# Optimization experiments

Hardware: AMD Instinct MI355X
Metric: run time of the kernel (lower is better)

## Reference

```python
import jax, jax.numpy as jnp
import numpy as np

B, MAX_S, HID = 128, 4096, 5120
H, D_NOPE, D_ROPE, D_V = 128, 128, 64, 128
KV_SIZE = 512 + 64  # kv_lora_rank + qk_rope_head_dim = 576


def setup_inputs() -> dict:
    key = jax.random.key(0)
    ks = jax.random.split(key, 8)
    seq_lens = jax.random.randint(ks[0], (B,), 1, MAX_S)
    return {
        "hidden_states": jax.random.normal(ks[1], (B, 1, HID), jnp.float32),
        "k_cache": jax.random.normal(ks[2], (B, MAX_S, D_NOPE), jnp.float32),
        "v_cache": jax.random.normal(ks[3], (B, MAX_S, D_V), jnp.float32),
        "Wq": jax.random.normal(ks[4], (HID, H * (D_NOPE + D_ROPE)), jnp.float32) * 0.02,
        "Wkv": jax.random.normal(ks[5], (HID, KV_SIZE), jnp.float32) * 0.02,
        "Wo": jax.random.normal(ks[6], (H * D_V, HID), jnp.float32) * 0.02,
        "positions": seq_lens - 1,
        "slot_mapping": seq_lens - 1,
        "seq_lens": seq_lens,
    }


def reference(hidden_states, k_cache, v_cache, Wq, Wkv, Wo, positions, slot_mapping, seq_lens):
    h = hidden_states[:, -1, :]                        # [B, HID] last-token decode
    q = (h @ Wq).reshape(B, H, D_NOPE + D_ROPE)        # [B, H, 192]
    kv = h @ Wkv                                       # [B, 576]
    q_nope = q[:, :, :D_NOPE]                          # [B, H, 128]
    k_new = kv[:, :D_NOPE]                             # [B, 128]
    v_new = kv[:, D_NOPE:D_NOPE + D_V]                 # [B, 128]

    b_idx = jnp.arange(B)
    kc = k_cache.at[b_idx, slot_mapping].set(k_new)    # write new token into paged cache
    vc = v_cache.at[b_idx, slot_mapping].set(v_new)

    scale = D_NOPE ** -0.5
    scores = jnp.einsum('bhd,bsd->bhs', q_nope, kc) * scale  # MQA: 1 kv head broadcast
    valid = jnp.arange(MAX_S)[None, :] < seq_lens[:, None]   # [B, S]
    scores = jnp.where(valid[:, None, :], scores, jnp.float32(-1e30))
    p = jax.nn.softmax(scores, axis=-1)
    attn = jnp.einsum('bhs,bsd->bhd', p, vc)           # [B, H, 128]

    return attn.reshape(B, 1, H * D_V) @ Wo            # [B, 1, HID]
```

## Files before the change

### kernel.cpp

```cpp
#include <hip/hip_runtime.h>
#include <hip/hip_bf16.h>

typedef __attribute__((ext_vector_type(4))) float f32x4;
typedef __attribute__((ext_vector_type(8))) short bf16x8;
typedef __attribute__((ext_vector_type(2))) unsigned int u32x2;
typedef __attribute__((ext_vector_type(4))) unsigned int u32x4;

static __device__ __forceinline__ unsigned short f2bf(float f) {
    unsigned u = __builtin_bit_cast(unsigned, f);
    u += 0x7fffu + ((u >> 16) & 1u);
    return (unsigned short)(u >> 16);
}
static __device__ __forceinline__ unsigned pack2(float a, float b) {
    __hip_bfloat162 h = __float22bfloat162_rn(make_float2(a, b));
    unsigned u;
    __builtin_memcpy(&u, &h, 4);
    return u;
}
static __device__ __forceinline__ float bf2f(unsigned short s) {
    unsigned u = (unsigned)s << 16;
    float f;
    __builtin_memcpy(&f, &u, 4);
    return f;
}

static __device__ __forceinline__ void bar_nodrain() {
    __builtin_amdgcn_sched_barrier(0);
    asm volatile("s_waitcnt lgkmcnt(0)" ::: "memory");
    __builtin_amdgcn_s_barrier();
    __builtin_amdgcn_sched_barrier(0);
}

__global__ __launch_bounds__(256)
void cvt_bf16(const float* __restrict__ in, unsigned* __restrict__ out, int n8)
{
    const int i = blockIdx.x * 256 + threadIdx.x;
    if (i >= n8) return;
    f32x4 a = ((const f32x4*)in)[2 * i];
    f32x4 b = ((const f32x4*)in)[2 * i + 1];
    u32x4 p = { pack2(a[0], a[1]), pack2(a[2], a[3]), pack2(b[0], b[1]), pack2(b[2], b[3]) };
    ((u32x4*)out)[i] = p;
}

template<int CBF16, int COLMAP>
__device__ __forceinline__
void gemm_body(const unsigned short* __restrict__ Ah, int lda,
               const float* __restrict__ Bm, int ldb,
               void* __restrict__ Cp, int ldc,
               int kchunk, int nsplit, int bidx,
               unsigned short* As, unsigned short* Bs)
{
    const int tid = threadIdx.x;
    const int w = tid >> 6, l = tid & 63, lg = l >> 4, l15 = l & 15;
    const int bx = bidx / nsplit;
    const int by = bidx % nsplit;
    const int n0 = bx * 64;
    const int pcol = COLMAP ? ((n0 >> 7) * 192 + (n0 & 127)) : n0;
    const size_t k0base = (size_t)by * (size_t)kchunk;

    const int ar = tid >> 1;
    const int ac = (tid & 1) * 32;
    const int bnb = (tid & 15) * 4;
    const int bkk = tid >> 4;

    u32x4 aReg[4];
    f32x4 b0Reg[2][2], b1Reg[2][2];

    auto loadA = [&](size_t k0) {
#pragma unroll
        for (int k = 0; k < 4; k++)
            aReg[k] = *(const u32x4*)(Ah + (size_t)ar * lda + k0 + ac + 8 * k);
    };
    auto storeA = [&]() {
#pragma unroll
        for (int k = 0; k < 4; k++)
            *(u32x4*)&As[ar * 72 + ac + 8 * k] = aReg[k];
    };
    auto loadB = [&](f32x4 (&bR)[2][2], size_t k0) {
#pragma unroll
        for (int i = 0; i < 2; i++) {
            const float* bp = Bm + (k0 + (size_t)(2 * (bkk + 16 * i))) * (size_t)ldb + pcol + bnb;
            bR[i][0] = *(const f32x4*)bp;
            bR[i][1] = *(const f32x4*)(bp + ldb);
        }
    };
    auto storeB = [&](f32x4 (&bR)[2][2]) {
        unsigned* bd = (unsigned*)Bs;
#pragma unroll
        for (int i = 0; i < 2; i++)
#pragma unroll
            for (int j = 0; j < 4; j++)
                bd[(bnb + j) * 33 + bkk + 16 * i] = pack2(bR[i][0][j], bR[i][1][j]);
    };

    f32x4 acc[2][4];
    const f32x4 fzero = {0.f, 0.f, 0.f, 0.f};
#pragma unroll
    for (int a = 0; a < 2; a++)
#pragma unroll
        for (int b2 = 0; b2 < 4; b2++) acc[a][b2] = fzero;

    auto mfmaStep = [&]() {
#pragma unroll
        for (int ks = 0; ks < 2; ks++) {
            bf16x8 bfr[4];
#pragma unroll
            for (int nf = 0; nf < 4; nf++)
                bfr[nf] = *(const bf16x8*)&Bs[(16 * nf + l15) * 66 + 32 * ks + 8 * lg];
#pragma unroll
            for (int mf = 0; mf < 2; mf++) {
                bf16x8 af = *(const bf16x8*)&As[(32 * w + 16 * mf + l15) * 72 + 32 * ks + 8 * lg];
#pragma unroll
                for (int nf = 0; nf < 4; nf++)
                    acc[mf][nf] = __builtin_amdgcn_mfma_f32_16x16x32_bf16(af, bfr[nf], acc[mf][nf], 0, 0, 0);
            }
        }
    };

    const int nst = kchunk >> 6;
    auto kof = [&](int t) { return k0base + (size_t)(t << 6); };

    loadA(kof(0));
    loadB(b0Reg, kof(0));
    if (nst > 1) loadB(b1Reg, kof(1));

    for (int t = 0; t < nst; t += 2) {
        storeA(); storeB(b0Reg);
        bar_nodrain();
        if (t + 1 < nst) loadA(kof(t + 1));
        if (t + 2 < nst) loadB(b0Reg, kof(t + 2));
        __builtin_amdgcn_sched_barrier(0);
        mfmaStep();
        bar_nodrain();
        if (t + 1 < nst) {
            storeA(); storeB(b1Reg);
            bar_nodrain();
            if (t + 2 < nst) loadA(kof(t + 2));
            if (t + 3 < nst) loadB(b1Reg, kof(t + 3));
            __builtin_amdgcn_sched_barrier(0);
            mfmaStep();
            bar_nodrain();
        }
    }
#pragma unroll
    for (int mf = 0; mf < 2; mf++) {
#pragma unroll
        for (int nf = 0; nf < 4; nf++) {
            const int m0 = 32 * w + 16 * mf + 4 * lg;
            const int cn = n0 + 16 * nf + l15;
            if (CBF16) {
                unsigned short* Ch = (unsigned short*)Cp + (size_t)by * ((size_t)128 * (size_t)ldc);
#pragma unroll
                for (int r = 0; r < 4; r++)
                    Ch[(size_t)(m0 + r) * ldc + cn] = f2bf(acc[mf][nf][r]);
            } else {
                float* Cf = (float*)Cp + (size_t)by * ((size_t)128 * (size_t)ldc);
#pragma unroll
                for (int r = 0; r < 4; r++)
                    Cf[(size_t)(m0 + r) * ldc + cn] = acc[mf][nf][r];
            }
        }
    }
}

#define QBLOCKS 1024

__global__ __launch_bounds__(256, 4)
void proj_fused(const unsigned short* __restrict__ hb,
                const float* __restrict__ Wq, const float* __restrict__ Wkv,
                unsigned short* __restrict__ qp, float* __restrict__ kvp)
{
    __shared__ __align__(16) unsigned short As[128 * 72];
    __shared__ __align__(16) unsigned short Bs[64 * 66];
    if (blockIdx.x < QBLOCKS)
        gemm_body<1, 1>(hb, 5120, Wq, 24576, qp, 16384, 1280, 4, blockIdx.x, As, Bs);
    else
        gemm_body<0, 0>(hb, 5120, Wkv, 576, kvp, 256, 320, 16, blockIdx.x - QBLOCKS, As, Bs);
}

__global__ __launch_bounds__(256, 4)
void gemm_out(const unsigned short* __restrict__ Ah, const float* __restrict__ Wo,
              unsigned short* __restrict__ outp)
{
    __shared__ __align__(16) unsigned short As[128 * 72];
    __shared__ __align__(16) unsigned short Bs[64 * 66];
    gemm_body<1, 0>(Ah, 16384, Wo, 5120, outp, 5120, 1024, 16, blockIdx.x, As, Bs);
}

__global__ __launch_bounds__(256)
void reduce_q_bf16(const unsigned short* __restrict__ in, unsigned* __restrict__ out)
{
    const int i = blockIdx.x * 256 + threadIdx.x;
    const u32x4* in4 = (const u32x4*)in;
    u32x4 v0 = in4[i];
    u32x4 v1 = in4[i + 262144];
    u32x4 v2 = in4[i + 2 * 262144];
    u32x4 v3 = in4[i + 3 * 262144];
    const float scale = 0.088388347648318447f;
    u32x4 r;
#pragma unroll
    for (int wd = 0; wd < 4; wd++) {
        float lo = bf2f((unsigned short)(v0[wd] & 0xffff)) + bf2f((unsigned short)(v1[wd] & 0xffff))
                 + bf2f((unsigned short)(v2[wd] & 0xffff)) + bf2f((unsigned short)(v3[wd] & 0xffff));
        float hi = bf2f((unsigned short)(v0[wd] >> 16)) + bf2f((unsigned short)(v1[wd] >> 16))
                 + bf2f((unsigned short)(v2[wd] >> 16)) + bf2f((unsigned short)(v3[wd] >> 16));
        r[wd] = pack2(lo * scale, hi * scale);
    }
    ((u32x4*)out)[i] = r;
}

#define NSPLIT 8
#define CHUNK_T 8
#define KVSPLIT 16

__global__ __launch_bounds__(512, 4)
void attn_fwd(const float* __restrict__ kc, const float* __restrict__ vc,
              const unsigned short* __restrict__ qb, const float* __restrict__ kvp,
              const int* __restrict__ seq_lens, const int* __restrict__ slot_map,
              unsigned short* __restrict__ Opart, float* __restrict__ m_ws, float* __restrict__ l_ws)
{
    __shared__ __align__(16) unsigned short Ks [64 * 136];
    __shared__ __align__(16) unsigned short Vts[128 * 72];
    __shared__ __align__(16) unsigned short Ps [128 * 72];
    __shared__ float knew_s[128];
    __shared__ float vnew_s[128];

    const int b = blockIdx.x, split = blockIdx.y;
    const int seq = seq_lens[b], slot = slot_map[b];
    const int nt = (seq + 63) >> 6;
    const int t0 = split * CHUNK_T;
    const int t1 = min(t0 + CHUNK_T, nt);
    const int slotTile = slot >> 6;

    const int tid = threadIdx.x, w = tid >> 6, l = tid & 63, lg = l >> 4, l15 = l & 15;
    const int h = 16 * w + l15;

    float m_run = -__builtin_inff(), l_run = 0.0f;

    if (t0 < t1) {
        if (slotTile >= t0 && slotTile < t1 && tid < 256) {
            float s = 0.f;
#pragma unroll
            for (int j = 0; j < KVSPLIT; j++) s += kvp[j * 32768 + b * 256 + tid];
            if (tid < 128) knew_s[tid] = s;
            else           vnew_s[tid - 128] = s;
        }

        bf16x8 qf[4];
        {
            const unsigned short* qrow = qb + (size_t)b * 16384 + (size_t)h * 128;
#pragma unroll
            for (int ks = 0; ks < 4; ks++)
                qf[ks] = *(const bf16x8*)(qrow + 32 * ks + 8 * lg);
        }

        f32x4 kReg[4];
        f32x4 vReg[2][2];
        const int kr  = tid >> 3;
        const int kcb = (tid & 7) * 16;
        const int vsp = tid & 31;
        const int vdq = tid >> 5;

        auto loadKV = [&](int t) {
            const int s0 = t << 6;
            const float* ksrc = kc + ((size_t)b * 4096 + s0 + kr) * 128 + kcb;
#pragma unroll
            for (int c = 0; c < 4; c++) kReg[c] = *(const f32x4*)(ksrc + 4 * c);
#pragma unroll
            for (int i = 0; i < 2; i++) {
                const int d4 = 4 * vdq + 64 * i;
                const float* r1 = vc + ((size_t)b * 4096 + s0 + 2 * vsp) * 128 + d4;
                vReg[i][0] = *(const f32x4*)r1;
                vReg[i][1] = *(const f32x4*)(r1 + 128);
            }
        };
        auto storeKV = [&]() {
            u32x4 w0 = { pack2(kReg[0][0], kReg[0][1]), pack2(kReg[0][2], kReg[0][3]),
                         pack2(kReg[1][0], kReg[1][1]), pack2(kReg[1][2], kReg[1][3]) };
            u32x4 w1 = { pack2(kReg[2][0], kReg[2][1]), pack2(kReg[2][2], kReg[2][3]),
                         pack2(kReg[3][0], kReg[3][1]), pack2(kReg[3][2], kReg[3][3]) };
            *(u32x4*)&Ks[kr * 136 + kcb] = w0;
            *(u32x4*)&Ks[kr * 136 + kcb + 8] = w1;
            unsigned* vt = (unsigned*)Vts;
#pragma unroll
            for (int i = 0; i < 2; i++)
#pragma unroll
                for (int j = 0; j < 4; j++)
                    vt[(4 * vdq + 64 * i + j) * 36 + vsp] = pack2(vReg[i][0][j], vReg[i][1][j]);
        };

        f32x4 accO[8];
        const f32x4 fzero = {0.f, 0.f, 0.f, 0.f};
#pragma unroll
        for (int i = 0; i < 8; i++) accO[i] = fzero;

        loadKV(t0);
        for (int t = t0; t < t1; ++t) {
            const int s0 = t << 6;
            storeKV();
            bar_nodrain();
            if (t == slotTile) {
                if (tid < 128) {
                    const int sloc = slot & 63;
                    Ks [sloc * 136 + tid] = f2bf(knew_s[tid]);
                    Vts[tid * 72 + sloc]  = f2bf(vnew_s[tid]);
                }
                bar_nodrain();
            }
            if (t + 1 < t1) loadKV(t + 1);
            __builtin_amdgcn_sched_barrier(0);

            f32x4 accS[4];
#pragma unroll
            for (int sf = 0; sf < 4; sf++) accS[sf] = fzero;
#pragma unroll
            for (int ks = 0; ks < 4; ks++) {
#pragma unroll
                for (int sf = 0; sf < 4; sf++) {
                    bf16x8 kf = *(const bf16x8*)&Ks[(16 * sf + l15) * 136 + 32 * ks + 8 * lg];
                    accS[sf] = __builtin_amdgcn_mfma_f32_16x16x32_bf16(kf, qf[ks], accS[sf], 0, 0, 0);
                }
            }
            float tmax = -__builtin_inff();
#pragma unroll
            for (int sf = 0; sf < 4; sf++) {
#pragma unroll
                for (int r = 0; r < 4; r++) {
                    const int s = s0 + 16 * sf + 4 * lg + r;
                    float sc = (s < seq) ? accS[sf][r] : -__builtin_inff();
                    accS[sf][r] = sc;
                    tmax = fmaxf(tmax, sc);
                }
            }
            tmax = fmaxf(tmax, __shfl_xor(tmax, 16));
            tmax = fmaxf(tmax, __shfl_xor(tmax, 32));
            const float mnew = fmaxf(m_run, tmax);
            const float so = __expf(m_run - mnew);
            float lsum = 0.f;
#pragma unroll
            for (int sf = 0; sf < 4; sf++) {
#pragma unroll
                for (int r = 0; r < 4; r++) {
                    const float p = __expf(accS[sf][r] - mnew);
                    accS[sf][r] = p;
                    lsum += p;
                }
            }
            lsum += __shfl_xor(lsum, 16);
            lsum += __shfl_xor(lsum, 32);
            l_run = l_run * so + lsum;
            m_run = mnew;
#pragma unroll
            for (int i = 0; i < 8; i++) accO[i] *= so;

            {
                unsigned* pd = (unsigned*)Ps;
#pragma unroll
                for (int sf = 0; sf < 4; sf++) {
                    pd[h * 36 + 8 * sf + 2 * lg + 0] = pack2(accS[sf][0], accS[sf][1]);
                    pd[h * 36 + 8 * sf + 2 * lg + 1] = pack2(accS[sf][2], accS[sf][3]);
                }
            }
            bf16x8 pf[2];
#pragma unroll
            for (int ks = 0; ks < 2; ks++)
                pf[ks] = *(const bf16x8*)&Ps[h * 72 + 32 * ks + 8 * lg];
#pragma unroll
            for (int df = 0; df < 8; df++) {
#pragma unroll
                for (int ks = 0; ks < 2; ks++) {
                    bf16x8 vf = *(const bf16x8*)&Vts[(16 * df + l15) * 72 + 32 * ks + 8 * lg];
                    accO[df] = __builtin_amdgcn_mfma_f32_16x16x32_bf16(vf, pf[ks], accO[df], 0, 0, 0);
                }
            }
            bar_nodrain();
        }
        unsigned short* ob = Opart + ((size_t)(b * NSPLIT + split)) * 16384 + (size_t)h * 128;
#pragma unroll
        for (int df = 0; df < 8; df++) {
            u32x2 p = { pack2(accO[df][0], accO[df][1]), pack2(accO[df][2], accO[df][3]) };
            *(u32x2*)&ob[16 * df + 4 * lg] = p;
        }
    }
    if (lg == 0) {
        m_ws[(b * NSPLIT + split) * 128 + h] = m_run;
        l_ws[(b * NSPLIT + split) * 128 + h] = l_run;
    }
}

__global__ __launch_bounds__(256)
void combine8(const unsigned short* __restrict__ Opart, const float* __restrict__ m_ws,
              const float* __restrict__ l_ws, unsigned* __restrict__ attn_bf)
{
    const int idx = blockIdx.x * 256 + threadIdx.x;
    const int d4 = (idx & 31) * 4;
    const int hh = (idx >> 5) & 127;
    const int b = idx >> 12;

    float m = -__builtin_inff();
    float mv[NSPLIT], lv[NSPLIT];
#pragma unroll
    for (int j = 0; j < NSPLIT; j++) {
        mv[j] = m_ws[(b * NSPLIT + j) * 128 + hh];
        lv[j] = l_ws[(b * NSPLIT + j) * 128 + hh];
        m = fmaxf(m, mv[j]);
    }
    f32x4 o = {0.f, 0.f, 0.f, 0.f};
    float lsum = 0.f;
#pragma unroll
    for (int j = 0; j < NSPLIT; j++) {
        const float a = (lv[j] > 0.f) ? __expf(mv[j] - m) : 0.f;
        lsum += a * lv[j];
        if (a > 0.f) {
            u32x2 v = *(const u32x2*)&Opart[((size_t)(b * NSPLIT + j)) * 16384 + (size_t)hh * 128 + d4];
            f32x4 oj = { bf2f((unsigned short)(v[0] & 0xffff)), bf2f((unsigned short)(v[0] >> 16)),
                         bf2f((unsigned short)(v[1] & 0xffff)), bf2f((unsigned short)(v[1] >> 16)) };
            o += oj * a;
        }
    }
    o *= (1.0f / lsum);
    u32x2 p = { pack2(o[0], o[1]), pack2(o[2], o[3]) };
    *(u32x2*)&attn_bf[(size_t)b * 8192 + (size_t)hh * 64 + (d4 >> 1)] = p;
}

__global__ __launch_bounds__(256)
void reduce_out_f32(const unsigned short* __restrict__ in, float* __restrict__ out)
{
    const int i = blockIdx.x * 256 + threadIdx.x;
    f32x4 s = {0.f, 0.f, 0.f, 0.f};
#pragma unroll
    for (int j = 0; j < 16; j++) {
        u32x2 v = *(const u32x2*)&in[(size_t)j * 655360 + 4 * (size_t)i];
        s[0] += bf2f((unsigned short)(v[0] & 0xffff));
        s[1] += bf2f((unsigned short)(v[0] >> 16));
        s[2] += bf2f((unsigned short)(v[1] & 0xffff));
        s[3] += bf2f((unsigned short)(v[1] >> 16));
    }
    ((f32x4*)out)[i] = s;
}

extern "C" void kernel_launch(void* const* d_in, const int* in_sizes, int n_in,
                              void* d_out, int out_size, void* d_ws, size_t ws_size,
                              hipStream_t stream)
{
    const float* hidden  = (const float*)d_in[0];
    const float* k_cache = (const float*)d_in[1];
    const float* v_cache = (const float*)d_in[2];
    const float* Wq      = (const float*)d_in[3];
    const float* Wkv     = (const float*)d_in[4];
    const float* Wo      = (const float*)d_in[5];
    const int* slot_map  = (const int*)d_in[7];
    const int* seq_lens  = (const int*)d_in[8];
    float* out = (float*)d_out;

    float* ws = (float*)d_ws;
    unsigned short* hb      = (unsigned short*)(ws);
    unsigned short* qp      = (unsigned short*)(ws + 327680);
    unsigned short* qb      = (unsigned short*)(ws + 4521984);
    float*          kvp     = ws + 5570560;
    unsigned short* attn_bf = (unsigned short*)(ws + 6094848);
    unsigned short* Opart   = (unsigned short*)(ws + 7143424);
    float*          m_ws    = ws + 15532032;
    float*          l_ws    = ws + 15663104;
    unsigned short* outp    = (unsigned short*)(ws + 15794176);

    cvt_bf16<<<dim3(320), 256, 0, stream>>>(hidden, (unsigned*)hb, 81920);
    proj_fused<<<dim3(QBLOCKS + 64), 256, 0, stream>>>(hb, Wq, Wkv, qp, kvp);
    reduce_q_bf16<<<dim3(1024), 256, 0, stream>>>(qp, (unsigned*)qb);
    attn_fwd<<<dim3(128, NSPLIT), 512, 0, stream>>>(k_cache, v_cache, qb, kvp,
                                                    seq_lens, slot_map, Opart, m_ws, l_ws);
    combine8<<<dim3(2048), 256, 0, stream>>>(Opart, m_ws, l_ws, (unsigned*)attn_bf);
    gemm_out<<<dim3(80 * 16), 256, 0, stream>>>(attn_bf, Wo, outp);
    reduce_out_f32<<<dim3(640), 256, 0, stream>>>(outp, out);
}
```

Measured before the change: 325.2 us.

## Widen GEMM N-tile to 128 columns and single-buffer B prefetch

Doubles the GEMM block tile width from 64 to 128 output columns, so each staged A tile is reused across twice as many MFMAs and half as many blocks are launched for the Q/KV projections and the output projection. The block index mapping changes to tile-major within each K split, and the two-register B double buffer is replaced by one larger register set with a simpler one-stage prefetch loop. Larger accumulators and shared memory lower occupancy (launch bounds drop to 3 blocks per CU), and the simpler loop may expose more load latency.

```diff
diff --git a/kernel.cpp b/kernel.cpp
--- a/kernel.cpp
+++ b/kernel.cpp
@@ -44,27 +44,27 @@
 
 template<int CBF16, int COLMAP>
 __device__ __forceinline__
-void gemm_body(const unsigned short* __restrict__ Ah, int lda,
-               const float* __restrict__ Bm, int ldb,
-               void* __restrict__ Cp, int ldc,
-               int kchunk, int nsplit, int bidx,
-               unsigned short* As, unsigned short* Bs)
+void gemm_body128(const unsigned short* __restrict__ Ah, int lda,
+                  const float* __restrict__ Bm, int ldb,
+                  void* __restrict__ Cp, int ldc,
+                  int kchunk, int ntiles, int bidx,
+                  unsigned short* As, unsigned short* Bs)
 {
     const int tid = threadIdx.x;
     const int w = tid >> 6, l = tid & 63, lg = l >> 4, l15 = l & 15;
-    const int bx = bidx / nsplit;
-    const int by = bidx % nsplit;
-    const int n0 = bx * 64;
-    const int pcol = COLMAP ? ((n0 >> 7) * 192 + (n0 & 127)) : n0;
+    const int bx = bidx % ntiles;
+    const int by = bidx / ntiles;
+    const int n0 = bx * 128;
+    const int pcol = COLMAP ? (bx * 192) : n0;
     const size_t k0base = (size_t)by * (size_t)kchunk;
 
     const int ar = tid >> 1;
     const int ac = (tid & 1) * 32;
-    const int bnb = (tid & 15) * 4;
-    const int bkk = tid >> 4;
+    const int bnb = (tid & 31) * 4;
+    const int bkk = tid >> 5;
 
     u32x4 aReg[4];
-    f32x4 b0Reg[2][2], b1Reg[2][2];
+    f32x4 bReg[4][2];
 
     auto loadA = [&](size_t k0) {
 #pragma unroll
@@ -76,76 +76,66 @@
         for (int k = 0; k < 4; k++)
             *(u32x4*)&As[ar * 72 + ac + 8 * k] = aReg[k];
     };
-    auto loadB = [&](f32x4 (&bR)[2][2], size_t k0) {
-#pragma unroll
-        for (int i = 0; i < 2; i++) {
-            const float* bp = Bm + (k0 + (size_t)(2 * (bkk + 16 * i))) * (size_t)ldb + pcol + bnb;
-            bR[i][0] = *(const f32x4*)bp;
-            bR[i][1] = *(const f32x4*)(bp + ldb);
+    auto loadB = [&](size_t k0) {
+#pragma unroll
+        for (int i = 0; i < 4; i++) {
+            const float* bp = Bm + (k0 + (size_t)(2 * (bkk + 8 * i))) * (size_t)ldb + pcol + bnb;
+            bReg[i][0] = *(const f32x4*)bp;
+            bReg[i][1] = *(const f32x4*)(bp + ldb);
         }
     };
-    auto storeB = [&](f32x4 (&bR)[2][2]) {
+    auto storeB = [&]() {
         unsigned* bd = (unsigned*)Bs;
 #pragma unroll
-        for (int i = 0; i < 2; i++)
+        for (int i = 0; i < 4; i++)
 #pragma unroll
             for (int j = 0; j < 4; j++)
-                bd[(bnb + j) * 33 + bkk + 16 * i] = pack2(bR[i][0][j], bR[i][1][j]);
+                bd[(bnb + j) * 33 + bkk + 8 * i] = pack2(bReg[i][0][j], bReg[i][1][j]);
     };
 
-    f32x4 acc[2][4];
+    f32x4 acc[2][8];
     const f32x4 fzero = {0.f, 0.f, 0.f, 0.f};
 #pragma unroll
     for (int a = 0; a < 2; a++)
 #pragma unroll
-        for (int b2 = 0; b2 < 4; b2++) acc[a][b2] = fzero;
+        for (int b2 = 0; b2 < 8; b2++) acc[a][b2] = fzero;
 
     auto mfmaStep = [&]() {
 #pragma unroll
         for (int ks = 0; ks < 2; ks++) {
-            bf16x8 bfr[4];
-#pragma unroll
-            for (int nf = 0; nf < 4; nf++)
+            bf16x8 bfr[8];
+#pragma unroll
+            for (int nf = 0; nf < 8; nf++)
                 bfr[nf] = *(const bf16x8*)&Bs[(16 * nf + l15) * 66 + 32 * ks + 8 * lg];
 #pragma unroll
             for (int mf = 0; mf < 2; mf++) {
                 bf16x8 af = *(const bf16x8*)&As[(32 * w + 16 * mf + l15) * 72 + 32 * ks + 8 * lg];
 #pragma unroll
-                for (int nf = 0; nf < 4; nf++)
+                for (int nf = 0; nf < 8; nf++)
                     acc[mf][nf] = __builtin_amdgcn_mfma_f32_16x16x32_bf16(af, bfr[nf], acc[mf][nf], 0, 0, 0);
             }
         }
     };
 
     const int nst = kchunk >> 6;
-    auto kof = [&](int t) { return k0base + (size_t)(t << 6); };
-
-    loadA(kof(0));
-    loadB(b0Reg, kof(0));
-    if (nst > 1) loadB(b1Reg, kof(1));
-
-    for (int t = 0; t < nst; t += 2) {
-        storeA(); storeB(b0Reg);
+    loadA(k0base);
+    loadB(k0base);
+
+    for (int t = 0; t < nst; ++t) {
+        storeA(); storeB();
         bar_nodrain();
-        if (t + 1 < nst) loadA(kof(t + 1));
-        if (t + 2 < nst) loadB(b0Reg, kof(t + 2));
+        if (t + 1 < nst) {
+            const size_t k0 = k0base + (size_t)((t + 1) << 6);
+            loadA(k0); loadB(k0);
+        }
         __builtin_amdgcn_sched_barrier(0);
         mfmaStep();
         bar_nodrain();
-        if (t + 1 < nst) {
-            storeA(); storeB(b1Reg);
-            bar_nodrain();
-            if (t + 2 < nst) loadA(kof(t + 2));
-            if (t + 3 < nst) loadB(b1Reg, kof(t + 3));
-            __builtin_amdgcn_sched_barrier(0);
-            mfmaStep();
-            bar_nodrain();
-        }
     }
 #pragma unroll
     for (int mf = 0; mf < 2; mf++) {
 #pragma unroll
-        for (int nf = 0; nf < 4; nf++) {
+        for (int nf = 0; nf < 8; nf++) {
             const int m0 = 32 * w + 16 * mf + 4 * lg;
             const int cn = n0 + 16 * nf + l15;
             if (CBF16) {
@@ -163,28 +153,28 @@
     }
 }
 
-#define QBLOCKS 1024
-
-__global__ __launch_bounds__(256, 4)
+#define QBLOCKS 512
+
+__global__ __launch_bounds__(256, 3)
 void proj_fused(const unsigned short* __restrict__ hb,
                 const float* __restrict__ Wq, const float* __restrict__ Wkv,
                 unsigned short* __restrict__ qp, float* __restrict__ kvp)
 {
     __shared__ __align__(16) unsigned short As[128 * 72];
-    __shared__ __align__(16) unsigned short Bs[64 * 66];
+    __shared__ __align__(16) unsigned short Bs[128 * 66];
     if (blockIdx.x < QBLOCKS)
-        gemm_body<1, 1>(hb, 5120, Wq, 24576, qp, 16384, 1280, 4, blockIdx.x, As, Bs);
+        gemm_body128<1, 1>(hb, 5120, Wq, 24576, qp, 16384, 1280, 128, blockIdx.x, As, Bs);
     else
-        gemm_body<0, 0>(hb, 5120, Wkv, 576, kvp, 256, 320, 16, blockIdx.x - QBLOCKS, As, Bs);
-}
-
-__global__ __launch_bounds__(256, 4)
+        gemm_body128<0, 0>(hb, 5120, Wkv, 576, kvp, 256, 320, 2, blockIdx.x - QBLOCKS, As, Bs);
+}
+
+__global__ __launch_bounds__(256, 3)
 void gemm_out(const unsigned short* __restrict__ Ah, const float* __restrict__ Wo,
               unsigned short* __restrict__ outp)
 {
     __shared__ __align__(16) unsigned short As[128 * 72];
-    __shared__ __align__(16) unsigned short Bs[64 * 66];
-    gemm_body<1, 0>(Ah, 16384, Wo, 5120, outp, 5120, 1024, 16, blockIdx.x, As, Bs);
+    __shared__ __align__(16) unsigned short Bs[128 * 66];
+    gemm_body128<1, 0>(Ah, 16384, Wo, 5120, outp, 5120, 1024, 40, blockIdx.x, As, Bs);
 }
 
 __global__ __launch_bounds__(256)
@@ -465,11 +455,11 @@
     unsigned short* outp    = (unsigned short*)(ws + 15794176);
 
     cvt_bf16<<<dim3(320), 256, 0, stream>>>(hidden, (unsigned*)hb, 81920);
-    proj_fused<<<dim3(QBLOCKS + 64), 256, 0, stream>>>(hb, Wq, Wkv, qp, kvp);
+    proj_fused<<<dim3(QBLOCKS + 32), 256, 0, stream>>>(hb, Wq, Wkv, qp, kvp);
     reduce_q_bf16<<<dim3(1024), 256, 0, stream>>>(qp, (unsigned*)qb);
     attn_fwd<<<dim3(128, NSPLIT), 512, 0, stream>>>(k_cache, v_cache, qb, kvp,
                                                     seq_lens, slot_map, Opart, m_ws, l_ws);
     combine8<<<dim3(2048), 256, 0, stream>>>(Opart, m_ws, l_ws, (unsigned*)attn_bf);
-    gemm_out<<<dim3(80 * 16), 256, 0, stream>>>(attn_bf, Wo, outp);
+    gemm_out<<<dim3(40 * 16), 256, 0, stream>>>(attn_bf, Wo, outp);
     reduce_out_f32<<<dim3(640), 256, 0, stream>>>(outp, out);
 }
```

Result: slower. 347.7 us (+6.9%).
